# Performance work log

Measured on AMD Instinct MI355X. Metric: run time of the kernel, lower is better.

Reference implementation:

```python
import jax, jax.numpy as jnp
import numpy as np

EPS = 1e-5
GROUPS = 4


def gconv1x1(x, w, b, groups):
    # x: [B,C,H,W]; w: [Cout, Cin//groups]; grouped 1x1 conv
    B, C, H, W = x.shape
    Co = w.shape[0]
    xg = x.reshape(B, groups, C // groups, H, W)
    wg = w.reshape(groups, Co // groups, C // groups)
    y = jnp.einsum('bgchw,goc->bgohw', xg, wg).reshape(B, Co, H, W)
    if b is not None:
        y = y + b[None, :, None, None]
    return y


def setup_inputs() -> dict:
    key = jax.random.key(0)
    ks = jax.random.split(key, 9)
    B, C, H, W = 8, 64, 160, 160
    Cq = C // 8
    s = 0.1
    return {
        'x': jax.random.normal(ks[0], (B, C, H, W), jnp.float32),
        'wq': jax.random.normal(ks[1], (Cq, C // GROUPS), jnp.float32) * s,
        'bq': jax.random.normal(ks[2], (Cq,), jnp.float32) * s,
        'wk': jax.random.normal(ks[3], (Cq, C // GROUPS), jnp.float32) * s,
        'bk': jax.random.normal(ks[4], (Cq,), jnp.float32) * s,
        'wv': jax.random.normal(ks[5], (C, C // GROUPS), jnp.float32) * s,
        'bv': jax.random.normal(ks[6], (C,), jnp.float32) * s,
        'gamma': jax.random.normal(ks[7], (1,), jnp.float32) * s,
        'w1d': jax.random.normal(ks[8], (C, C // GROUPS), jnp.float32) * s,
        'bn_w': jnp.ones((C,), jnp.float32),
        'bn_b': jnp.zeros((C,), jnp.float32),
    }


def reference(x, wq, bq, wk, bk, wv, bv, gamma, w1d, bn_w, bn_b):
    B, C, H, W = x.shape
    q = gconv1x1(x, wq, bq, GROUPS)   # [B,Cq,H,W]
    k = gconv1x1(x, wk, bk, GROUPS)   # [B,Cq,H,W]
    v = gconv1x1(x, wv, bv, GROUPS)   # [B,C,H,W]

    # column (H) attention energies with -inf diagonal (self excluded on H path)
    energy_H = jnp.einsum('bchw,bcjw->bhwj', q, k)  # [B,H,W,H]
    diag = jnp.where(jnp.eye(H, dtype=bool), -jnp.inf, 0.0).astype(x.dtype)
    energy_H = energy_H + diag[:, None, :]
    # row (W) attention energies
    energy_W = jnp.einsum('bchw,bchj->bhwj', q, k)  # [B,H,W,W]

    att = jax.nn.softmax(jnp.concatenate([energy_H, energy_W], axis=3), axis=3)
    att_H = att[..., :H]           # [B,H,W,H]
    att_W = att[..., H:]           # [B,H,W,W]

    out_H = jnp.einsum('bcjw,bhwj->bchw', v, att_H)
    out_W = jnp.einsum('bchj,bhwj->bchw', v, att_W)
    out = gamma[0] * (out_H + out_W)               # [B,C,H,W]

    # kernel-size-1 grouped conv1d (dilation irrelevant for k=1), no bias
    L = H * W
    o = out.reshape(B, GROUPS, C // GROUPS, L)
    w1g = w1d.reshape(GROUPS, C // GROUPS, C // GROUPS)
    o = jnp.einsum('bgcl,goc->bgol', o, w1g).reshape(B, C, L)

    # BatchNorm1d (training mode: batch stats over (B, L), biased variance)
    mean = jnp.mean(o, axis=(0, 2), keepdims=True)
    var = jnp.mean((o - mean) ** 2, axis=(0, 2), keepdims=True)
    o = (o - mean) / jnp.sqrt(var + EPS) * bn_w[None, :, None] + bn_b[None, :, None]

    o = o.reshape(B, C, H, W)
    return jax.nn.relu(o + x)
```

## Files before the change

kernel.cpp:

```cpp
#include <hip/hip_runtime.h>
#include <math.h>

#define B_ 8
#define C_ 64
#define H_ 160
#define W_ 160
#define HW_ (H_*W_)

typedef _Float16 h2 __attribute__((ext_vector_type(2)));
typedef _Float16 h8 __attribute__((ext_vector_type(8)));
typedef float f4v __attribute__((ext_vector_type(4)));
union H8u { h8 v; h2 h[4]; };

__device__ inline float fdot2(h2 a, h2 b, float c) {
    return __builtin_amdgcn_fdot2(a, b, c, false);
}
__device__ inline float dot16(const float4* xr, const float* wr, float acc) {
    float4 a = xr[0], b = xr[1], c = xr[2], d = xr[3];
    acc += a.x*wr[0]  + a.y*wr[1]  + a.z*wr[2]  + a.w*wr[3];
    acc += b.x*wr[4]  + b.y*wr[5]  + b.z*wr[6]  + b.w*wr[7];
    acc += c.x*wr[8]  + c.y*wr[9]  + c.z*wr[10] + c.w*wr[11];
    acc += d.x*wr[12] + d.y*wr[13] + d.z*wr[14] + d.w*wr[15];
    return acc;
}

static constexpr size_t N_PIX  = (size_t)B_*H_*W_;
static constexpr size_t N_FULL = (size_t)B_*H_*W_*C_;
static constexpr size_t OFF_OUTH  = 0;
static constexpr size_t OFF_VROW  = N_FULL/2;
static constexpr size_t OFF_QROW  = OFF_VROW + N_FULL/2;
static constexpr size_t OFF_KROW  = OFF_QROW + N_PIX*4;
static constexpr size_t OFF_MH    = OFF_KROW + N_PIX*4;
static constexpr size_t OFF_SH    = OFF_MH + N_PIX;
static constexpr size_t OFF_BNSUM = OFF_SH + N_PIX;
static constexpr size_t OFF_BNSQ  = OFF_BNSUM + 64;

__global__ __launch_bounds__(256,4) void qkv_kernel(
    const float* __restrict__ x,
    const float* __restrict__ wq, const float* __restrict__ bq,
    const float* __restrict__ wk, const float* __restrict__ bk,
    const float* __restrict__ wv, const float* __restrict__ bv,
    _Float16* __restrict__ qrow, _Float16* __restrict__ krow,
    _Float16* __restrict__ vrow)
{
    __shared__ __align__(16) float xs[128][68];
    const int tid = threadIdx.x;
    const int w0 = blockIdx.x * 32;
    const int h0 = blockIdx.y * 4;
    const int b  = blockIdx.z;

    const float* xb = x + (size_t)b*C_*HW_;
    for (int i = tid; i < 2048; i += 256) {
        int w4 = i & 7;
        int c  = ((i >> 3) & 7) | (((i >> 6) & 7) << 3);
        int hh = i >> 9;
        float4 v = *(const float4*)(xb + (size_t)c*HW_ + (size_t)(h0+hh)*W_ + w0 + w4*4);
        int pix = hh*32 + w4*4;
        xs[pix+0][c] = v.x; xs[pix+1][c] = v.y; xs[pix+2][c] = v.z; xs[pix+3][c] = v.w;
    }
    __syncthreads();

    float resv[32];
    {
        const int cp = tid & 31, pg = tid >> 5;
        const int c0 = 2*cp, g = c0 >> 4;
        float w0r[16], w1r[16];
        #pragma unroll
        for (int p = 0; p < 4; p++) {
            *(float4*)&w0r[4*p] = ((const float4*)(wv + c0*16))[p];
            *(float4*)&w1r[4*p] = ((const float4*)(wv + (c0+1)*16))[p];
        }
        const float b0 = bv[c0], b1 = bv[c0+1];
        #pragma unroll 4
        for (int i = 0; i < 16; i++) {
            int pix = pg*16 + i;
            const float4* xr = (const float4*)&xs[pix][g*16];
            resv[2*i]   = dot16(xr, w0r, b0);
            resv[2*i+1] = dot16(xr, w1r, b1);
        }
    }
    float resqk[8];
    {
        const int out = tid & 15, pg = tid >> 4;
        const int cq = out & 7, g = cq >> 1;
        const float* wp = ((out < 8) ? wq : wk) + cq*16;
        const float bb = (out < 8) ? bq[cq] : bk[cq];
        float wr[16];
        #pragma unroll
        for (int p = 0; p < 4; p++) *(float4*)&wr[4*p] = ((const float4*)wp)[p];
        #pragma unroll
        for (int i = 0; i < 8; i++) {
            int pix = pg*8 + i;
            resqk[i] = dot16((const float4*)&xs[pix][g*16], wr, bb);
        }
    }
    __syncthreads();

    unsigned* vs32 = (unsigned*)&xs[0][0];
    unsigned* qk32 = vs32 + 4096;
    {
        const int cp = tid & 31, pg = tid >> 5;
        #pragma unroll
        for (int i = 0; i < 16; i++) {
            int pix = pg*16 + i;
            h2 p; p.x = (_Float16)resv[2*i]; p.y = (_Float16)resv[2*i+1];
            vs32[pix*32 + cp] = *(unsigned*)&p;
        }
    }
    {
        const int out = tid & 15, pg = tid >> 4;
        _Float16* qks = (_Float16*)qk32;
        #pragma unroll
        for (int i = 0; i < 8; i++) qks[(pg*8+i)*16 + out] = (_Float16)resqk[i];
    }
    __syncthreads();

    unsigned* vrow32 = (unsigned*)vrow;
    for (int i = tid; i < 4096; i += 256) {
        int pix = i >> 5, cp = i & 31;
        size_t bp = ((size_t)b*H_ + h0 + (pix>>5))*W_ + w0 + (pix & 31);
        vrow32[bp*32 + cp] = vs32[i];
    }
    unsigned* qrow32 = (unsigned*)qrow;
    unsigned* krow32 = (unsigned*)krow;
    for (int i = tid; i < 1024; i += 256) {
        int pix = i >> 3, part = i & 7;
        size_t bp = ((size_t)b*H_ + h0 + (pix>>5))*W_ + w0 + (pix & 31);
        unsigned val = qk32[pix*8 + part];
        if (part < 4) qrow32[bp*4 + part]     = val;
        else          krow32[bp*4 + part - 4] = val;
    }
}

__global__ __launch_bounds__(256,4) void passA_kernel(
    const _Float16* __restrict__ qrow, const _Float16* __restrict__ krow,
    const _Float16* __restrict__ vrow,
    _Float16* __restrict__ outH, float* __restrict__ mH, float* __restrict__ sH)
{
    __shared__ __align__(16) _Float16 v2s[5*4*64*8];
    __shared__ __align__(16) _Float16 Pts[5*4*32*8];
    __shared__ __align__(16) _Float16 q2h[160][8];
    __shared__ __align__(16) _Float16 k2h[160][8];

    const int tid = threadIdx.x;
    const int b = blockIdx.x / W_;
    const int w = blockIdx.x % W_;

    if (tid < 160) {
        size_t bp = ((size_t)b*H_ + tid)*W_ + w;
        *(int4*)&q2h[tid][0] = *(const int4*)(qrow + bp*8);
        *(int4*)&k2h[tid][0] = *(const int4*)(krow + bp*8);
    }
    {
        const unsigned* vr32 = (const unsigned*)vrow;
        const int cp = tid & 31, hp0 = tid >> 5;
        #pragma unroll 2
        for (int it = 0; it < 10; it++) {
            int hp = hp0 + 8*it;
            int kt = hp >> 4, dqv = (hp >> 2) & 3, jj = 2*(hp & 3);
            size_t bp0 = ((size_t)b*H_ + 2*hp)*W_ + w;
            unsigned u0 = vr32[bp0*32 + cp];
            unsigned u1 = vr32[(bp0 + W_)*32 + cp];
            unsigned e  = __builtin_amdgcn_perm(u1, u0, 0x05040100);
            unsigned o  = __builtin_amdgcn_perm(u1, u0, 0x07060302);
            int base = ((kt*4 + dqv)*64 + 2*cp)*8 + jj;
            *(unsigned*)&v2s[base]     = e;
            *(unsigned*)&v2s[base + 8] = o;
        }
    }
    __syncthreads();

    const int u    = tid & 7;
    const int wl   = tid >> 3;
    const int lane = tid & 63;
    const int wid  = tid >> 6;
    const int cM   = wid*16 + (lane & 15);
    const int m_   = lane & 15;
    const int dq   = lane >> 4;

    for (int t = 0; t < 5; t++) {
        const int qh = t*32 + wl;
        H8u qr; qr.v = *(const h8*)&q2h[qh][0];
        float ev[20];
        float mloc = -1e30f;
        #pragma unroll 2
        for (int p = 0; p < 10; p++) {
            int j0 = 2*u + 16*p;
            H8u ka; ka.v = *(const h8*)&k2h[j0][0];
            H8u kb; kb.v = *(const h8*)&k2h[j0+1][0];
            float e0 = 0.f, e1 = 0.f;
            #pragma unroll
            for (int i = 0; i < 4; i++) {
                e0 = fdot2(qr.h[i], ka.h[i], e0);
                e1 = fdot2(qr.h[i], kb.h[i], e1);
            }
            ev[2*p] = e0; ev[2*p+1] = e1;
            if (j0   != qh) mloc = fmaxf(mloc, e0);
            if (j0+1 != qh) mloc = fmaxf(mloc, e1);
        }
        mloc = fmaxf(mloc, __shfl_xor(mloc, 1));
        mloc = fmaxf(mloc, __shfl_xor(mloc, 2));
        mloc = fmaxf(mloc, __shfl_xor(mloc, 4));
        float sloc = 0.f;
        #pragma unroll
        for (int p = 0; p < 10; p++) {
            int j0 = 2*u + 16*p;
            float p0 = (j0   == qh) ? 0.f : __expf(ev[2*p]   - mloc);
            float p1 = (j0+1 == qh) ? 0.f : __expf(ev[2*p+1] - mloc);
            sloc += p0 + p1;
            h2 pp; pp.x = (_Float16)p0; pp.y = (_Float16)p1;
            int idx = (((p>>1)*4 + (u>>2) + 2*(p&1))*32 + wl)*8 + 2*(u&3);
            *(unsigned*)&Pts[idx] = *(unsigned*)&pp;
        }
        sloc += __shfl_xor(sloc, 1);
        sloc += __shfl_xor(sloc, 2);
        sloc += __shfl_xor(sloc, 4);
        if (u == 0) {
            mH[((size_t)b*W_ + w)*H_ + qh] = mloc;
            sH[((size_t)b*W_ + w)*H_ + qh] = sloc;
        }
        __syncthreads();

        f4v acc0 = {0.f,0.f,0.f,0.f}, acc1 = {0.f,0.f,0.f,0.f};
        #pragma unroll
        for (int kt = 0; kt < 5; kt++) {
            h8 bfr = *(const h8*)&v2s[((kt*4 + dq)*64 + cM)*8];
            h8 a0  = *(const h8*)&Pts[((kt*4 + dq)*32 + m_)*8];
            h8 a1  = *(const h8*)&Pts[((kt*4 + dq)*32 + 16 + m_)*8];
            acc0 = __builtin_amdgcn_mfma_f32_16x16x32_f16(a0, bfr, acc0, 0, 0, 0);
            acc1 = __builtin_amdgcn_mfma_f32_16x16x32_f16(a1, bfr, acc1, 0, 0, 0);
        }
        #pragma unroll
        for (int r = 0; r < 4; r++) {
            int r0 = t*32 + dq*4 + r;
            outH[(((size_t)b*H_ + r0     )*W_ + w)*64 + cM] = (_Float16)acc0[r];
            outH[(((size_t)b*H_ + r0 + 16)*W_ + w)*64 + cM] = (_Float16)acc1[r];
        }
        __syncthreads();
    }
}

__global__ __launch_bounds__(256,4) void passB_kernel(
    const _Float16* __restrict__ qrow, const _Float16* __restrict__ krow,
    const _Float16* vrow,
    const float* __restrict__ gamma, const float* __restrict__ w1d,
    const _Float16* __restrict__ outH, const float* __restrict__ mH, const float* __restrict__ sH,
    _Float16* o16, float* __restrict__ bnsum, float* __restrict__ bnsq)
{
    __shared__ __align__(16) _Float16 v2s[5*4*64*8];
    __shared__ __align__(16) _Float16 Pts[5*4*32*8];
    __shared__ __align__(16) _Float16 q2h[160][8];
    __shared__ __align__(16) _Float16 k2h[160][8];
    __shared__ __align__(16) _Float16 stageh[4*32*18];
    __shared__ float fHs[32], fWs[32];

    const int tid = threadIdx.x;
    const int b = blockIdx.x / H_;
    const int h = blockIdx.x % H_;
    const float gam = gamma[0];

    const int lane = tid & 63;
    const int wid  = tid >> 6;
    const int cM   = wid*16 + (lane & 15);
    const int m_   = lane & 15;
    const int dq   = lane >> 4;

    h2 w1h[8];
    #pragma unroll
    for (int p = 0; p < 8; p++) {
        float2 wpair = ((const float2*)(w1d + cM*16))[p];
        h2 wp; wp.x = (_Float16)wpair.x; wp.y = (_Float16)wpair.y;
        w1h[p] = wp;
    }

    const size_t rowbase = ((size_t)b*H_ + h)*W_;
    if (tid < 160) {
        size_t bp = rowbase + tid;
        *(int4*)&q2h[tid][0] = *(const int4*)(qrow + bp*8);
        *(int4*)&k2h[tid][0] = *(const int4*)(krow + bp*8);
    }
    {
        const unsigned* vr32 = (const unsigned*)vrow;
        const int cp = tid & 31, wp0 = tid >> 5;
        #pragma unroll 2
        for (int it = 0; it < 10; it++) {
            int wp = wp0 + 8*it;
            int kt = wp >> 4, dqv = (wp >> 2) & 3, jj = 2*(wp & 3);
            size_t bp0 = rowbase + 2*wp;
            unsigned u0 = vr32[bp0*32 + cp];
            unsigned u1 = vr32[(bp0 + 1)*32 + cp];
            unsigned e  = __builtin_amdgcn_perm(u1, u0, 0x05040100);
            unsigned o  = __builtin_amdgcn_perm(u1, u0, 0x07060302);
            int base = ((kt*4 + dqv)*64 + 2*cp)*8 + jj;
            *(unsigned*)&v2s[base]     = e;
            *(unsigned*)&v2s[base + 8] = o;
        }
    }
    __syncthreads();

    const int u  = tid & 7;
    const int wl = tid >> 3;
    float bnS = 0.f, bnS2 = 0.f;

    for (int t = 0; t < 5; t++) {
        float oh0[4], oh1[4];
        #pragma unroll
        for (int r = 0; r < 4; r++) {
            int rw0 = t*32 + dq*4 + r;
            oh0[r] = (float)outH[(rowbase + rw0     )*64 + cM];
            oh1[r] = (float)outH[(rowbase + rw0 + 16)*64 + cM];
        }

        const int qw = t*32 + wl;
        H8u qr; qr.v = *(const h8*)&q2h[qw][0];
        float ev[20];
        float mloc = -1e30f;
        #pragma unroll 2
        for (int p = 0; p < 10; p++) {
            int j0 = 2*u + 16*p;
            H8u ka; ka.v = *(const h8*)&k2h[j0][0];
            H8u kb; kb.v = *(const h8*)&k2h[j0+1][0];
            float e0 = 0.f, e1 = 0.f;
            #pragma unroll
            for (int i = 0; i < 4; i++) {
                e0 = fdot2(qr.h[i], ka.h[i], e0);
                e1 = fdot2(qr.h[i], kb.h[i], e1);
            }
            ev[2*p] = e0; ev[2*p+1] = e1;
            mloc = fmaxf(mloc, e0);
            mloc = fmaxf(mloc, e1);
        }
        mloc = fmaxf(mloc, __shfl_xor(mloc, 1));
        mloc = fmaxf(mloc, __shfl_xor(mloc, 2));
        mloc = fmaxf(mloc, __shfl_xor(mloc, 4));
        float sloc = 0.f;
        #pragma unroll
        for (int p = 0; p < 10; p++) {
            float p0 = __expf(ev[2*p]   - mloc);
            float p1 = __expf(ev[2*p+1] - mloc);
            sloc += p0 + p1;
            h2 pp; pp.x = (_Float16)p0; pp.y = (_Float16)p1;
            int idx = (((p>>1)*4 + (u>>2) + 2*(p&1))*32 + wl)*8 + 2*(u&3);
            *(unsigned*)&Pts[idx] = *(unsigned*)&pp;
        }
        sloc += __shfl_xor(sloc, 1);
        sloc += __shfl_xor(sloc, 2);
        sloc += __shfl_xor(sloc, 4);
        if (u == 0) {
            float mHv = mH[((size_t)b*W_ + qw)*H_ + h];
            float sHv = sH[((size_t)b*W_ + qw)*H_ + h];
            float M   = fmaxf(mHv, mloc);
            float eH  = __expf(mHv - M), eW = __expf(mloc - M);
            float inv = gam / (sHv*eH + sloc*eW);
            fHs[wl] = eH * inv;
            fWs[wl] = eW * inv;
        }
        __syncthreads();

        f4v acc0 = {0.f,0.f,0.f,0.f}, acc1 = {0.f,0.f,0.f,0.f};
        #pragma unroll
        for (int kt = 0; kt < 5; kt++) {
            h8 bfr = *(const h8*)&v2s[((kt*4 + dq)*64 + cM)*8];
            h8 a0  = *(const h8*)&Pts[((kt*4 + dq)*32 + m_)*8];
            h8 a1  = *(const h8*)&Pts[((kt*4 + dq)*32 + 16 + m_)*8];
            acc0 = __builtin_amdgcn_mfma_f32_16x16x32_f16(a0, bfr, acc0, 0, 0, 0);
            acc1 = __builtin_amdgcn_mfma_f32_16x16x32_f16(a1, bfr, acc1, 0, 0, 0);
        }
        _Float16* st = &stageh[wid*576];
        #pragma unroll
        for (int r = 0; r < 4; r++) {
            int rl0 = dq*4 + r, rl1 = rl0 + 16;
            st[rl0*18 + m_] = (_Float16)(oh0[r]*fHs[rl0] + acc0[r]*fWs[rl0]);
            st[rl1*18 + m_] = (_Float16)(oh1[r]*fHs[rl1] + acc1[r]*fWs[rl1]);
        }
        #pragma unroll
        for (int r = 0; r < 4; r++) {
            #pragma unroll
            for (int mt = 0; mt < 2; mt++) {
                int rl = dq*4 + r + 16*mt;
                int rw = t*32 + rl;
                const h2* sp = (const h2*)&st[rl*18];
                float o = 0.f;
                #pragma unroll
                for (int p = 0; p < 8; p++) o = fdot2(sp[p], w1h[p], o);
                o16[(rowbase + rw)*64 + cM] = (_Float16)o;
                bnS  += o;
                bnS2 += o*o;
            }
        }
        __syncthreads();
    }
    bnS  += __shfl_xor(bnS, 16);  bnS  += __shfl_xor(bnS, 32);
    bnS2 += __shfl_xor(bnS2, 16); bnS2 += __shfl_xor(bnS2, 32);
    if (dq == 0) {
        atomicAdd(&bnsum[cM], bnS);
        atomicAdd(&bnsq[cM],  bnS2);
    }
}

__global__ __launch_bounds__(256) void final_kernel(
    const float* __restrict__ x, const _Float16* __restrict__ o16,
    const float* __restrict__ bnsum, const float* __restrict__ bnsq,
    const float* __restrict__ bn_w, const float* __restrict__ bn_b,
    float* __restrict__ out)
{
    __shared__ _Float16 olds[160*66];
    __shared__ float sc[64], sh[64];
    const int tid = threadIdx.x;
    const int b = blockIdx.x / H_, h = blockIdx.x % H_;
    if (tid < 64) {
        const float cnt = (float)(B_*H_*W_);
        float mean = bnsum[tid] / cnt;
        float var  = bnsq[tid] / cnt - mean*mean;
        float istd = rsqrtf(var + 1e-5f);
        float scl  = bn_w[tid] * istd;
        sc[tid] = scl;
        sh[tid] = bn_b[tid] - mean*scl;
    }
    const unsigned* op = (const unsigned*)(o16 + ((size_t)b*H_ + h)*W_*64);
    unsigned* ol32 = (unsigned*)olds;
    for (int i = tid; i < 5120; i += 256) {
        int w = i >> 5, c2 = i & 31;
        ol32[w*33 + c2] = op[i];
    }
    __syncthreads();
    const float* xr = x   + (size_t)b*C_*HW_ + (size_t)h*W_;
    float*       ob = out + (size_t)b*C_*HW_ + (size_t)h*W_;
    for (int i = tid; i < 64*160; i += 256) {
        int c = i / 160, w = i - c*160;
        float v = (float)olds[w*66 + c] * sc[c] + sh[c] + xr[(size_t)c*HW_ + w];
        ob[(size_t)c*HW_ + w] = fmaxf(v, 0.f);
    }
}

extern "C" void kernel_launch(void* const* d_in, const int* in_sizes, int n_in,
                              void* d_out, int out_size, void* d_ws, size_t ws_size,
                              hipStream_t stream)
{
    (void)in_sizes; (void)n_in; (void)out_size; (void)ws_size;
    const float* x     = (const float*)d_in[0];
    const float* wq    = (const float*)d_in[1];
    const float* bq    = (const float*)d_in[2];
    const float* wk    = (const float*)d_in[3];
    const float* bk    = (const float*)d_in[4];
    const float* wv    = (const float*)d_in[5];
    const float* bv    = (const float*)d_in[6];
    const float* gamma = (const float*)d_in[7];
    const float* w1d   = (const float*)d_in[8];
    const float* bn_w  = (const float*)d_in[9];
    const float* bn_b  = (const float*)d_in[10];

    float* ws = (float*)d_ws;
    _Float16* outH16 = (_Float16*)(ws + OFF_OUTH);
    _Float16* vrow   = (_Float16*)(ws + OFF_VROW);
    _Float16* qrow   = (_Float16*)(ws + OFF_QROW);
    _Float16* krow   = (_Float16*)(ws + OFF_KROW);
    float* mH    = ws + OFF_MH;
    float* sH    = ws + OFF_SH;
    float* bnsum = ws + OFF_BNSUM;
    float* bnsq  = ws + OFF_BNSQ;
    _Float16* o16 = vrow;

    hipMemsetAsync(bnsum, 0, 128*sizeof(float), stream);

    dim3 qgrid(W_/32, H_/4, B_);
    qkv_kernel<<<qgrid, 256, 0, stream>>>(x, wq, bq, wk, bk, wv, bv, qrow, krow, vrow);
    passA_kernel<<<B_*W_, 256, 0, stream>>>(qrow, krow, vrow, outH16, mH, sH);
    passB_kernel<<<B_*H_, 256, 0, stream>>>(qrow, krow, vrow, gamma, w1d,
                                            outH16, mH, sH, o16, bnsum, bnsq);
    final_kernel<<<B_*H_, 256, 0, stream>>>(x, o16, bnsum, bnsq, bn_w, bn_b, (float*)d_out);
}
```

Before: 246.1 us.

## Hoist V fragments into registers and alias LDS buffers to raise occupancy

Both attention passes now load their V MFMA B-fragments from LDS into registers once, then reuse the same LDS region for the P tile (and the stage buffer in passB). This shrinks the shared-memory footprint, so launch bounds go from 4 to 5 blocks per SM. In passB the outH loads move after the softmax to shorten their live range. The cost is 20 extra VGPRs per thread for the fragments, which could cause spills under the tighter 5-block register budget.

```diff
diff --git a/kernel.cpp b/kernel.cpp
--- a/kernel.cpp
+++ b/kernel.cpp
@@ -132,15 +132,17 @@
     }
 }
 
-__global__ __launch_bounds__(256,4) void passA_kernel(
+__global__ __launch_bounds__(256,5) void passA_kernel(
     const _Float16* __restrict__ qrow, const _Float16* __restrict__ krow,
     const _Float16* __restrict__ vrow,
     _Float16* __restrict__ outH, float* __restrict__ mH, float* __restrict__ sH)
 {
-    __shared__ __align__(16) _Float16 v2s[5*4*64*8];
-    __shared__ __align__(16) _Float16 Pts[5*4*32*8];
+    __shared__ __align__(16) _Float16 pool[10240];
     __shared__ __align__(16) _Float16 q2h[160][8];
     __shared__ __align__(16) _Float16 k2h[160][8];
+
+    _Float16* v2s = pool;
+    _Float16* Pts = pool;
 
     const int tid = threadIdx.x;
     const int b = blockIdx.x / W_;
@@ -177,6 +179,12 @@
     const int cM   = wid*16 + (lane & 15);
     const int m_   = lane & 15;
     const int dq   = lane >> 4;
+
+    h8 vfr[5];
+    #pragma unroll
+    for (int kt = 0; kt < 5; kt++)
+        vfr[kt] = *(const h8*)&v2s[((kt*4 + dq)*64 + cM)*8];
+    __syncthreads();
 
     for (int t = 0; t < 5; t++) {
         const int qh = t*32 + wl;
@@ -224,11 +232,10 @@
         f4v acc0 = {0.f,0.f,0.f,0.f}, acc1 = {0.f,0.f,0.f,0.f};
         #pragma unroll
         for (int kt = 0; kt < 5; kt++) {
-            h8 bfr = *(const h8*)&v2s[((kt*4 + dq)*64 + cM)*8];
             h8 a0  = *(const h8*)&Pts[((kt*4 + dq)*32 + m_)*8];
             h8 a1  = *(const h8*)&Pts[((kt*4 + dq)*32 + 16 + m_)*8];
-            acc0 = __builtin_amdgcn_mfma_f32_16x16x32_f16(a0, bfr, acc0, 0, 0, 0);
-            acc1 = __builtin_amdgcn_mfma_f32_16x16x32_f16(a1, bfr, acc1, 0, 0, 0);
+            acc0 = __builtin_amdgcn_mfma_f32_16x16x32_f16(a0, vfr[kt], acc0, 0, 0, 0);
+            acc1 = __builtin_amdgcn_mfma_f32_16x16x32_f16(a1, vfr[kt], acc1, 0, 0, 0);
         }
         #pragma unroll
         for (int r = 0; r < 4; r++) {
@@ -240,19 +247,21 @@
     }
 }
 
-__global__ __launch_bounds__(256,4) void passB_kernel(
+__global__ __launch_bounds__(256,5) void passB_kernel(
     const _Float16* __restrict__ qrow, const _Float16* __restrict__ krow,
     const _Float16* vrow,
     const float* __restrict__ gamma, const float* __restrict__ w1d,
     const _Float16* __restrict__ outH, const float* __restrict__ mH, const float* __restrict__ sH,
     _Float16* o16, float* __restrict__ bnsum, float* __restrict__ bnsq)
 {
-    __shared__ __align__(16) _Float16 v2s[5*4*64*8];
-    __shared__ __align__(16) _Float16 Pts[5*4*32*8];
+    __shared__ __align__(16) _Float16 pool[10240];
     __shared__ __align__(16) _Float16 q2h[160][8];
     __shared__ __align__(16) _Float16 k2h[160][8];
-    __shared__ __align__(16) _Float16 stageh[4*32*18];
     __shared__ float fHs[32], fWs[32];
+
+    _Float16* v2s    = pool;
+    _Float16* Pts    = pool;
+    _Float16* stageh = pool + 5120;
 
     const int tid = threadIdx.x;
     const int b = blockIdx.x / H_;
@@ -300,17 +309,16 @@
 
     const int u  = tid & 7;
     const int wl = tid >> 3;
+
+    h8 vfr[5];
+    #pragma unroll
+    for (int kt = 0; kt < 5; kt++)
+        vfr[kt] = *(const h8*)&v2s[((kt*4 + dq)*64 + cM)*8];
+    __syncthreads();
+
     float bnS = 0.f, bnS2 = 0.f;
 
     for (int t = 0; t < 5; t++) {
-        float oh0[4], oh1[4];
-        #pragma unroll
-        for (int r = 0; r < 4; r++) {
-            int rw0 = t*32 + dq*4 + r;
-            oh0[r] = (float)outH[(rowbase + rw0     )*64 + cM];
-            oh1[r] = (float)outH[(rowbase + rw0 + 16)*64 + cM];
-        }
-
         const int qw = t*32 + wl;
         H8u qr; qr.v = *(const h8*)&q2h[qw][0];
         float ev[20];
@@ -355,16 +363,22 @@
             fHs[wl] = eH * inv;
             fWs[wl] = eW * inv;
         }
+        float oh0[4], oh1[4];
+        #pragma unroll
+        for (int r = 0; r < 4; r++) {
+            int rw0 = t*32 + dq*4 + r;
+            oh0[r] = (float)outH[(rowbase + rw0     )*64 + cM];
+            oh1[r] = (float)outH[(rowbase + rw0 + 16)*64 + cM];
+        }
         __syncthreads();
 
         f4v acc0 = {0.f,0.f,0.f,0.f}, acc1 = {0.f,0.f,0.f,0.f};
         #pragma unroll
         for (int kt = 0; kt < 5; kt++) {
-            h8 bfr = *(const h8*)&v2s[((kt*4 + dq)*64 + cM)*8];
             h8 a0  = *(const h8*)&Pts[((kt*4 + dq)*32 + m_)*8];
             h8 a1  = *(const h8*)&Pts[((kt*4 + dq)*32 + 16 + m_)*8];
-            acc0 = __builtin_amdgcn_mfma_f32_16x16x32_f16(a0, bfr, acc0, 0, 0, 0);
-            acc1 = __builtin_amdgcn_mfma_f32_16x16x32_f16(a1, bfr, acc1, 0, 0, 0);
+            acc0 = __builtin_amdgcn_mfma_f32_16x16x32_f16(a0, vfr[kt], acc0, 0, 0, 0);
+            acc1 = __builtin_amdgcn_mfma_f32_16x16x32_f16(a1, vfr[kt], acc1, 0, 0, 0);
         }
         _Float16* st = &stageh[wid*576];
         #pragma unroll
```

Measured after the change: 278.3 us. +13.1%, slower.
